# Kernel tuning notes

Measured on AMD Instinct MI355X. Metric: run time of the kernel, lower is better.

Reference implementation:

```python
import jax, jax.numpy as jnp
import numpy as np


def _forward(q, k, Wq, bq, Wk, bk, Wp, bp, eps=1e-4):
    b, ck, hk, wk, dk = k.shape
    n = hk * wk * dk                      # k sequence length == per-block q tokens
    # k branch: flatten spatial, project 256 -> 32
    kf = jnp.einsum('bci,cd->bid', k.reshape(b, ck, n), Wk) + bk   # (b, n, C)
    k_norm = jnp.linalg.norm(kf, axis=1)                           # (b, C): norm over positions (torch dim=1)
    c = q.shape[1]
    hq, wq, dq = q.shape[2], q.shape[3], q.shape[4]
    Nq = hq * wq * dq
    qf = jnp.einsum('bci,cd->bid', q.reshape(b, c, Nq), Wq) + bq   # (b, Nq, C)
    C = qf.shape[-1]
    Bh, Bw, Bd = hq // hk, wq // wk, dq // dk
    G = Bh * Bw * Bd
    # gather all (h_k, w_k, d_k) blocks: (b, G, n, C) -- replaces triple python loop
    qb = (qf.reshape(b, Bh, hk, Bw, wk, Bd, dk, C)
            .transpose(0, 1, 3, 5, 2, 4, 6, 7)
            .reshape(b, G, n, C))
    q_norm = jnp.linalg.norm(qb, axis=2)                           # (b, G, C): per-channel norm over block positions
    denom = jnp.einsum('bc,bgc->bg', k_norm, q_norm) + eps         # scalar per (batch, block)
    # sim[b,g,j,i] = <kf[b,i,:], qb[b,g,j,:]> / denom  (already in post-permute layout)
    sim = jnp.einsum('bic,bgjc->bgji', kf, qb) / denom[:, :, None, None]
    att = jax.nn.softmax(sim, axis=-1)                             # softmax over k positions i
    out = jnp.einsum('bgji,bgic->bgjc', att, qb)                   # (b, G, n, C)
    # min-max renorm over positions within each block (torch dim=1 of (b,n,C))
    mn = out.min(axis=2, keepdims=True)
    mx = out.max(axis=2, keepdims=True)
    v = (out - mn) / (mx - mn + eps)
    # faithful torch reshape: (b, C, n) row-major reinterpreted as (b, hk, wk, dk, C)
    v = v.transpose(0, 1, 3, 2).reshape(b, Bh, Bw, Bd, hk, wk, dk, C)
    # scatter blocks back to full volume
    v = v.transpose(0, 1, 4, 2, 5, 3, 6, 7).reshape(b, hq, wq, dq, C)
    out = jnp.einsum('bhwdc,ce->bhwde', v, Wp) + bp
    return out.transpose(0, 4, 1, 2, 3)                            # (b, C, hq, wq, dq)


def setup_inputs() -> dict:
    key = jax.random.key(0)
    ks = jax.random.split(key, 8)
    nf = 16
    q = jax.random.normal(ks[0], (2, nf * 2, 32, 32, 32), jnp.float32)
    k = jax.random.normal(ks[1], (2, nf * 16, 8, 8, 8), jnp.float32)
    Wq = jax.random.normal(ks[2], (nf * 2, nf * 2), jnp.float32) * 0.05
    bq = jax.random.normal(ks[3], (nf * 2,), jnp.float32) * 0.05
    Wk = jax.random.normal(ks[4], (nf * 16, nf * 2), jnp.float32) * 0.05
    bk = jax.random.normal(ks[5], (nf * 2,), jnp.float32) * 0.05
    Wp = jax.random.normal(ks[6], (nf * 2, nf * 2), jnp.float32) * 0.05
    bp = jax.random.normal(ks[7], (nf * 2,), jnp.float32) * 0.05
    return {"q": q, "k": k, "Wq": Wq, "bq": bq, "Wk": Wk, "bk": bk, "Wp": Wp, "bp": bp}


def reference(q, k, Wq, bq, Wk, bk, Wp, bp):
    return _forward(q, k, Wq, bq, Wk, bk, Wp, bp)
```

## Files before the change

kernel.cpp:

```cpp
#include <hip/hip_runtime.h>
#include <hip/hip_bf16.h>
#include <cstdint>

typedef __attribute__((ext_vector_type(8))) short bf16x8;
typedef __attribute__((ext_vector_type(4))) float f32x4;

static __device__ __forceinline__ float lo16(uint32_t u){ return __uint_as_float(u << 16); }
static __device__ __forceinline__ float hi16(uint32_t u){ return __uint_as_float(u & 0xffff0000u); }
static __device__ __forceinline__ uint32_t f2bf(float x){
    uint32_t u = __float_as_uint(x);
    return (u + 0x7fffu + ((u >> 16) & 1u)) >> 16;
}
static __device__ __forceinline__ uint32_t pack2(float a, float b){
    return f2bf(a) | (f2bf(b) << 16);
}

__global__ __launch_bounds__(1024) void k_kf(const float* __restrict__ k,
    const float* __restrict__ Wk, const float* __restrict__ bk,
    uint32_t* __restrict__ kf_pack)
{
    __shared__ float Wk_s[8192];
    __shared__ float bk_s[32];
    __shared__ float red[32][32];
    int t = threadIdx.x;
    for (int L = t; L < 8192; L += 1024) Wk_s[L] = Wk[L];
    if (t < 32) bk_s[t] = bk[t];
    __syncthreads();
    int blk = blockIdx.x;
    int b = blk >> 7, i0 = (blk & 127) * 4;
    int d = t & 31, sub = t >> 5;
    int i = i0 + (sub >> 3);
    int cp = sub & 7;
    const float* kb = k + (size_t)b * 131072;
    float acc = 0.f;
    #pragma unroll 8
    for (int cc = 0; cc < 32; ++cc){
        int c = cp*32 + cc;
        acc += kb[c*512 + i] * Wk_s[c*32 + d];
    }
    red[sub][d] = acc;
    __syncthreads();
    if (t < 128){
        int isel = t >> 5, dd = t & 31;
        float s = bk_s[dd];
        #pragma unroll
        for (int cp2 = 0; cp2 < 8; ++cp2) s += red[isel*8 + cp2][dd];
        float sO = __shfl_xor(s, 1, 64);
        if ((dd & 1) == 0)
            kf_pack[(b*512 + i0 + isel)*16 + (dd >> 1)] = pack2(s, sO);
    }
}

__global__ __launch_bounds__(1024) void k_qb(const float* __restrict__ q,
    const float* __restrict__ Wq, const float* __restrict__ bq,
    uint32_t* __restrict__ qb_pack)
{
    __shared__ float Wq_s[1024], bq_s[32], q_s[8192];
    int t = threadIdx.x;
    int blk = blockIdx.x;
    int bg = blk >> 1, h = blk & 1;
    int b = bg >> 6, g = bg & 63;
    int bh = g >> 4, bw = (g >> 2) & 3, bd = g & 3;
    Wq_s[t & 1023] = Wq[t & 1023];
    if (t < 32) bq_s[t] = bq[t];
    const float* qbase = q + (size_t)b * 1048576;
    #pragma unroll
    for (int m = 0; m < 2; ++m){
        int L4 = m*1024 + t;
        int f4 = L4 & 1, iw = (L4 >> 1) & 7, ihl = (L4 >> 4) & 3, c = L4 >> 6;
        const float* src = qbase + c*32768 + (bh*8 + h*4 + ihl)*1024
                         + (bw*8 + iw)*32 + bd*8 + f4*4;
        float4 v = *(const float4*)src;
        *(float4*)&q_s[c*256 + ihl*64 + iw*8 + f4*4] = v;
    }
    __syncthreads();
    int d = t & 31, sub = t >> 5;
    uint32_t* qb_out = qb_pack + (size_t)bg * 8192 + h*4096;
    for (int it = 0; it < 8; ++it){
        int jl = it*32 + sub;
        float acc = bq_s[d];
        #pragma unroll
        for (int c = 0; c < 32; ++c)
            acc += q_s[c*256 + jl] * Wq_s[c*32 + d];
        float accO = __shfl_xor(acc, 1, 64);
        if ((d & 1) == 0) qb_out[jl*16 + (d >> 1)] = pack2(acc, accO);
    }
}

__global__ __launch_bounds__(1024) void k_attn_mfma(const uint32_t* __restrict__ kf_pack,
    const uint32_t* __restrict__ qb_pack,
    float* __restrict__ oraw, float* __restrict__ mnp, float* __restrict__ mxp)
{
    __shared__ uint32_t kfs32[8192];
    __shared__ uint16_t qbV16[16384];
    __shared__ uint16_t Ps16[16384];
    __shared__ float mred[16][64];
    __shared__ float stat[64][32];
    __shared__ float dens[16][16];
    __shared__ float knsh[32], vssh[32], dsh[32];
    __shared__ float denom_s;
    int t = threadIdx.x;
    int blk = blockIdx.x;
    int bg = blk >> 1, jhalf = blk & 1;
    int b = bg >> 6;
    {
        const uint32_t* src = kf_pack + b*8192;
        #pragma unroll
        for (int m = 0; m < 8; ++m){
            int flat = m*1024 + t;
            uint32_t v = src[flat];
            int i = flat >> 4, dp = flat & 15;
            kfs32[i*16 + (((dp>>2) ^ (i&3)) & 3)*4 + (dp&3)] = v;
        }
    }
    {
        const uint32_t* src = qb_pack + (size_t)bg*8192;
        #pragma unroll
        for (int m = 0; m < 8; ++m){
            int flat = m*1024 + t;
            int i = flat >> 4, dp = flat & 15;
            uint32_t v = src[flat];
            int d0 = 2*dp, d1 = 2*dp + 1;
            qbV16[d0*512 + (((i>>3) ^ (d0&7)) & 63)*8 + (i&7)] = (uint16_t)(v & 0xffffu);
            qbV16[d1*512 + (((i>>3) ^ (d1&7)) & 63)*8 + (i&7)] = (uint16_t)(v >> 16);
        }
    }
    __syncthreads();
    {
        int dp = t & 15, ig = t >> 4;
        float lo2 = 0.f, hi2 = 0.f;
        #pragma unroll
        for (int ii = 0; ii < 8; ++ii){
            int i = ig*8 + ii;
            uint32_t u = kfs32[i*16 + (((dp>>2) ^ (i&3)) & 3)*4 + (dp&3)];
            float a = lo16(u), c = hi16(u);
            lo2 += a*a; hi2 += c*c;
        }
        stat[ig][dp*2] = lo2; stat[ig][dp*2+1] = hi2;
    }
    __syncthreads();
    if (t < 32){
        float s = 0.f;
        #pragma unroll
        for (int u = 0; u < 64; ++u) s += stat[u][t];
        knsh[t] = s;
    }
    __syncthreads();
    {
        int d = t & 31, ig = t >> 5;
        float q2 = 0.f, vs = 0.f;
        #pragma unroll
        for (int ii = 0; ii < 16; ii += 2){
            int i = ig*16 + ii;
            uint32_t u = *(__shared__ uint32_t*)&qbV16[d*512 + (((i>>3) ^ (d&7)) & 63)*8 + (i&7)];
            float a = lo16(u), c = hi16(u);
            q2 += a*a + c*c; vs += a + c;
        }
        stat[ig][d] = q2; stat[32 + ig][d] = vs;
    }
    __syncthreads();
    if (t < 32){
        float q2 = 0.f, vs = 0.f;
        #pragma unroll
        for (int u = 0; u < 32; ++u){ q2 += stat[u][t]; vs += stat[32+u][t]; }
        vssh[t] = vs;
        dsh[t] = sqrtf(knsh[t]) * sqrtf(q2);
    }
    __syncthreads();
    if (t == 0){
        float s = 0.f;
        #pragma unroll
        for (int d2 = 0; d2 < 32; ++d2) s += dsh[d2];
        denom_s = s + 1e-4f;
    }
    __syncthreads();
    float rden = 1.0f / denom_s;
    int wave = t >> 6, lane = t & 63;
    int ln15 = lane & 15, quad = lane >> 4;
    uint16_t* Pw = Ps16 + wave*1024;
    float vs0[4], vs1[4];
    #pragma unroll
    for (int r = 0; r < 4; ++r){
        vs0[r] = vssh[quad*4 + r];
        vs1[r] = vssh[16 + quad*4 + r];
    }
    float* obase = oraw + (size_t)bg * 16384;
    int jloc = wave*16 + ln15;
    int jglob = jhalf*256 + jloc;
    union { bf16x8 v; uint16_t u[8]; } afr;
    #pragma unroll
    for (int jj = 0; jj < 8; ++jj){
        int d = quad*8 + jj;
        afr.u[jj] = qbV16[d*512 + (((jglob>>3) ^ (d&7)) & 63)*8 + (jglob&7)];
    }
    f32x4 pv0 = {0.f,0.f,0.f,0.f}, pv1 = {0.f,0.f,0.f,0.f};
    float pdn[4] = {0.f,0.f,0.f,0.f};
    for (int sb = 0; sb < 4; ++sb){
        f32x4 sacc[8];
        #pragma unroll
        for (int u = 0; u < 8; ++u){
            int i = sb*128 + u*16 + ln15;
            bf16x8 bfr = *(__shared__ bf16x8*)&kfs32[i*16 + ((quad ^ (i&3)) & 3)*4];
            f32x4 z = {0.f,0.f,0.f,0.f};
            sacc[u] = __builtin_amdgcn_mfma_f32_16x16x32_bf16(afr.v, bfr, z, 0, 0, 0);
        }
        #pragma unroll
        for (int h2 = 0; h2 < 2; ++h2){
            #pragma unroll
            for (int u4 = 0; u4 < 4; ++u4){
                int u = h2*4 + u4;
                int il = u4*16 + ln15;
                #pragma unroll
                for (int r = 0; r < 4; ++r){
                    float x = sacc[u][r] * rden;
                    float e = x + x*x*(0.5f + x*(1.0f/6.0f));
                    pdn[r] += e;
                    int jrow = quad*4 + r;
                    Pw[jrow*64 + (((il>>3) ^ (jrow&3)) & 7)*8 + (il&7)] = (uint16_t)f2bf(e);
                }
            }
            __threadfence_block();
            #pragma unroll
            for (int ks = 0; ks < 2; ++ks){
                int i0 = ks*32 + quad*8;
                bf16x8 bp = *(__shared__ bf16x8*)&Pw[ln15*64 + (((i0>>3) ^ (ln15&3)) & 7)*8];
                int ig = sb*128 + h2*64 + i0;
                int c0 = ln15, c1 = 16 + ln15;
                bf16x8 av0 = *(__shared__ bf16x8*)&qbV16[c0*512 + (((ig>>3) ^ (c0&7)) & 63)*8];
                bf16x8 av1 = *(__shared__ bf16x8*)&qbV16[c1*512 + (((ig>>3) ^ (c1&7)) & 63)*8];
                pv0 = __builtin_amdgcn_mfma_f32_16x16x32_bf16(av0, bp, pv0, 0, 0, 0);
                pv1 = __builtin_amdgcn_mfma_f32_16x16x32_bf16(av1, bp, pv1, 0, 0, 0);
            }
        }
    }
    #pragma unroll
    for (int r = 0; r < 4; ++r){
        float s = pdn[r];
        s += __shfl_xor(s, 1, 64);
        s += __shfl_xor(s, 2, 64);
        s += __shfl_xor(s, 4, 64);
        s += __shfl_xor(s, 8, 64);
        if (ln15 == 0) dens[wave][quad*4 + r] = s;
    }
    __threadfence_block();
    float rl = 1.0f / (512.f + dens[wave][ln15]);
    float o0[4], o1[4];
    #pragma unroll
    for (int r = 0; r < 4; ++r){
        o0[r] = (vs0[r] + pv0[r]) * rl;
        o1[r] = (vs1[r] + pv1[r]) * rl;
        obase[(quad*4 + r)*512 + jglob]      = o0[r];
        obase[(16 + quad*4 + r)*512 + jglob] = o1[r];
    }
    #pragma unroll
    for (int r = 0; r < 4; ++r){
        float mnA = o0[r], mxA = o0[r], mnB = o1[r], mxB = o1[r];
        #pragma unroll
        for (int off = 1; off < 16; off <<= 1){
            mnA = fminf(mnA, __shfl_xor(mnA, off, 64));
            mxA = fmaxf(mxA, __shfl_xor(mxA, off, 64));
            mnB = fminf(mnB, __shfl_xor(mnB, off, 64));
            mxB = fmaxf(mxB, __shfl_xor(mxB, off, 64));
        }
        if (ln15 == 0){
            mred[wave][quad*4 + r]      = mnA;
            mred[wave][32 + quad*4 + r] = mxA;
            mred[wave][16 + quad*4 + r] = mnB;
            mred[wave][48 + quad*4 + r] = mxB;
        }
    }
    __syncthreads();
    if (t < 32){
        float mn = 3e38f, mx = -3e38f;
        #pragma unroll
        for (int w = 0; w < 16; ++w){
            mn = fminf(mn, mred[w][t]);
            mx = fmaxf(mx, mred[w][32 + t]);
        }
        int slot = (bg*2 + jhalf)*32 + t;
        mnp[slot] = mn;
        mxp[slot] = mx;
    }
}

__global__ __launch_bounds__(256) void k_proj(const float* __restrict__ oraw,
    const float* __restrict__ mnp, const float* __restrict__ mxp,
    const float* __restrict__ Wp, const float* __restrict__ bp,
    float* __restrict__ out)
{
    __shared__ float Wp_s[1024], bp_s[32];
    __shared__ float sh_v[32][32];
    __shared__ float sh_o[32][33];
    int t = threadIdx.x;
    if (t < 32) bp_s[t] = bp[t];
    for (int L = t; L < 1024; L += 256) Wp_s[L] = Wp[L];
    int blk = blockIdx.x;
    int b = blk >> 10, p0 = (blk & 1023) * 32;
    int c = t & 31, ip0 = t >> 5;
    float vv[4];
    #pragma unroll
    for (int m = 0; m < 4; ++m){
        int p = p0 + m*8 + ip0;
        int h = p >> 10, w = (p >> 5) & 31, dsp = p & 31;
        int f = (h >> 3)*262144 + (w >> 3)*65536 + (dsp >> 3)*16384
              + (h & 7)*2048 + (w & 7)*256 + (dsp & 7)*32;
        int flat = f + c;
        int cidx = b*2048 + (flat >> 9);
        int s0 = ((cidx >> 5) << 6) + (cidx & 31);
        float o  = oraw[(size_t)b*1048576 + flat];
        float mn = fminf(mnp[s0], mnp[s0 + 32]);
        float mx = fmaxf(mxp[s0], mxp[s0 + 32]);
        vv[m] = (o - mn) / (mx - mn + 1e-4f);
    }
    __syncthreads();
    #pragma unroll
    for (int m = 0; m < 4; ++m) sh_v[m*8 + ip0][c] = vv[m];
    __syncthreads();
    #pragma unroll
    for (int m = 0; m < 4; ++m){
        int pos = m*8 + ip0;
        float acc = bp_s[c];
        #pragma unroll
        for (int cc = 0; cc < 32; ++cc)
            acc += sh_v[pos][cc] * Wp_s[cc*32 + c];
        sh_o[pos][c] = acc;
    }
    __syncthreads();
    #pragma unroll
    for (int m = 0; m < 4; ++m){
        int e = m*8 + (t >> 5), pi = t & 31;
        out[((size_t)(b*32 + e) << 15) + p0 + pi] = sh_o[pi][e];
    }
}

extern "C" void kernel_launch(void* const* d_in, const int* in_sizes, int n_in,
                              void* d_out, int out_size, void* d_ws, size_t ws_size,
                              hipStream_t stream)
{
    const float* q  = (const float*)d_in[0];
    const float* k  = (const float*)d_in[1];
    const float* Wq = (const float*)d_in[2];
    const float* bq = (const float*)d_in[3];
    const float* Wk = (const float*)d_in[4];
    const float* bk = (const float*)d_in[5];
    const float* Wp = (const float*)d_in[6];
    const float* bp = (const float*)d_in[7];

    float* base      = (float*)d_ws;
    uint32_t* kf_pack = (uint32_t*)base;
    uint32_t* qb_pack = (uint32_t*)(base + 16384);
    float* oraw      = base + 1064960;
    float* mnp       = base + 3162112;
    float* mxp       = base + 3170304;
    float* outp      = (float*)d_out;

    hipLaunchKernelGGL(k_kf,        dim3(256),  dim3(1024), 0, stream, k, Wk, bk, kf_pack);
    hipLaunchKernelGGL(k_qb,        dim3(256),  dim3(1024), 0, stream, q, Wq, bq, qb_pack);
    hipLaunchKernelGGL(k_attn_mfma, dim3(256),  dim3(1024), 0, stream, kf_pack, qb_pack, oraw, mnp, mxp);
    hipLaunchKernelGGL(k_proj,      dim3(2048), dim3(256), 0, stream, oraw, mnp, mxp, Wp, bp, outp);
}
```

Measured before the change: 127.4 us.

## Merge projection kernels, keep softmax probabilities in registers via permlane swaps, split attention finer

The separate k and q projection kernels are merged into one launch that branches on block index. The q projection caches Wq columns in registers and computes four positions per thread. In attention, the score MFMA operands are swapped so the exponentiated scores can be packed with v_cvt_pk_bf16_f32 and rearranged with permlane32/16 swaps straight into the B operand of the PV MFMA, dropping the LDS round-trip for P and its buffer. Attention now runs 512 blocks of 512 threads with four query quarters, so min/max partials grow to four slots and k_proj reduces over them. The cost is recomputing the k-norm and q statistics in twice as many blocks, and relying on gfx950-specific instructions.

```diff
diff --git a/kernel.cpp b/kernel.cpp
--- a/kernel.cpp
+++ b/kernel.cpp
@@ -14,100 +14,127 @@
 static __device__ __forceinline__ uint32_t pack2(float a, float b){
     return f2bf(a) | (f2bf(b) << 16);
 }
-
-__global__ __launch_bounds__(1024) void k_kf(const float* __restrict__ k,
+static __device__ __forceinline__ uint32_t cvtpk(float a, float b){
+    uint32_t r;
+    asm("v_cvt_pk_bf16_f32 %0, %1, %2" : "=v"(r) : "v"(a), "v"(b));
+    return r;
+}
+static __device__ __forceinline__ void pl32swap(uint32_t &x, uint32_t &y){
+    asm("v_permlane32_swap_b32 %0, %1" : "+v"(x), "+v"(y));
+}
+static __device__ __forceinline__ void pl16swap(uint32_t &x, uint32_t &y){
+    asm("v_permlane16_swap_b32 %0, %1" : "+v"(x), "+v"(y));
+}
+
+__global__ __launch_bounds__(1024) void k_pre(const float* __restrict__ q,
+    const float* __restrict__ k,
+    const float* __restrict__ Wq, const float* __restrict__ bq,
     const float* __restrict__ Wk, const float* __restrict__ bk,
-    uint32_t* __restrict__ kf_pack)
+    uint32_t* __restrict__ qb_pack, uint32_t* __restrict__ kf_pack)
 {
-    __shared__ float Wk_s[8192];
-    __shared__ float bk_s[32];
-    __shared__ float red[32][32];
-    int t = threadIdx.x;
-    for (int L = t; L < 8192; L += 1024) Wk_s[L] = Wk[L];
-    if (t < 32) bk_s[t] = bk[t];
-    __syncthreads();
-    int blk = blockIdx.x;
-    int b = blk >> 7, i0 = (blk & 127) * 4;
-    int d = t & 31, sub = t >> 5;
-    int i = i0 + (sub >> 3);
-    int cp = sub & 7;
-    const float* kb = k + (size_t)b * 131072;
-    float acc = 0.f;
-    #pragma unroll 8
-    for (int cc = 0; cc < 32; ++cc){
-        int c = cp*32 + cc;
-        acc += kb[c*512 + i] * Wk_s[c*32 + d];
-    }
-    red[sub][d] = acc;
-    __syncthreads();
-    if (t < 128){
-        int isel = t >> 5, dd = t & 31;
-        float s = bk_s[dd];
-        #pragma unroll
-        for (int cp2 = 0; cp2 < 8; ++cp2) s += red[isel*8 + cp2][dd];
-        float sO = __shfl_xor(s, 1, 64);
-        if ((dd & 1) == 0)
-            kf_pack[(b*512 + i0 + isel)*16 + (dd >> 1)] = pack2(s, sO);
-    }
-}
-
-__global__ __launch_bounds__(1024) void k_qb(const float* __restrict__ q,
-    const float* __restrict__ Wq, const float* __restrict__ bq,
-    uint32_t* __restrict__ qb_pack)
-{
-    __shared__ float Wq_s[1024], bq_s[32], q_s[8192];
+    __shared__ float buf[9248];
     int t = threadIdx.x;
     int blk = blockIdx.x;
-    int bg = blk >> 1, h = blk & 1;
-    int b = bg >> 6, g = bg & 63;
-    int bh = g >> 4, bw = (g >> 2) & 3, bd = g & 3;
-    Wq_s[t & 1023] = Wq[t & 1023];
-    if (t < 32) bq_s[t] = bq[t];
-    const float* qbase = q + (size_t)b * 1048576;
-    #pragma unroll
-    for (int m = 0; m < 2; ++m){
-        int L4 = m*1024 + t;
-        int f4 = L4 & 1, iw = (L4 >> 1) & 7, ihl = (L4 >> 4) & 3, c = L4 >> 6;
-        const float* src = qbase + c*32768 + (bh*8 + h*4 + ihl)*1024
-                         + (bw*8 + iw)*32 + bd*8 + f4*4;
-        float4 v = *(const float4*)src;
-        *(float4*)&q_s[c*256 + ihl*64 + iw*8 + f4*4] = v;
-    }
-    __syncthreads();
-    int d = t & 31, sub = t >> 5;
-    uint32_t* qb_out = qb_pack + (size_t)bg * 8192 + h*4096;
-    for (int it = 0; it < 8; ++it){
-        int jl = it*32 + sub;
-        float acc = bq_s[d];
-        #pragma unroll
-        for (int c = 0; c < 32; ++c)
-            acc += q_s[c*256 + jl] * Wq_s[c*32 + d];
-        float accO = __shfl_xor(acc, 1, 64);
-        if ((d & 1) == 0) qb_out[jl*16 + (d >> 1)] = pack2(acc, accO);
-    }
-}
-
-__global__ __launch_bounds__(1024) void k_attn_mfma(const uint32_t* __restrict__ kf_pack,
+    if (blk < 256){
+        float* Wq_s = buf;
+        float* bq_s = buf + 1024;
+        float* q_s  = buf + 1056;
+        int bg = blk >> 1, h = blk & 1;
+        int b = bg >> 6, g = bg & 63;
+        int bh = g >> 4, bw = (g >> 2) & 3, bd = g & 3;
+        Wq_s[t] = Wq[t];
+        if (t < 32) bq_s[t] = bq[t];
+        const float* qbase = q + (size_t)b * 1048576;
+        #pragma unroll
+        for (int m = 0; m < 2; ++m){
+            int L4 = m*1024 + t;
+            int f4 = L4 & 1, iw = (L4 >> 1) & 7, ihl = (L4 >> 4) & 3, c = L4 >> 6;
+            const float* src = qbase + c*32768 + (bh*8 + h*4 + ihl)*1024
+                             + (bw*8 + iw)*32 + bd*8 + f4*4;
+            float4 v = *(const float4*)src;
+            *(float4*)&q_s[c*256 + ihl*64 + iw*8 + f4*4] = v;
+        }
+        __syncthreads();
+        int d = t & 31, sub = t >> 5;
+        float wq[32];
+        #pragma unroll
+        for (int c = 0; c < 32; ++c) wq[c] = Wq_s[c*32 + d];
+        uint32_t* qb_out = qb_pack + (size_t)bg * 8192 + h*4096;
+        #pragma unroll
+        for (int it = 0; it < 2; ++it){
+            int jl = it*128 + sub*4;
+            float bb = bq_s[d];
+            float a0 = bb, a1 = bb, a2 = bb, a3 = bb;
+            #pragma unroll
+            for (int c = 0; c < 32; ++c){
+                float4 qv = *(const float4*)&q_s[c*256 + jl];
+                a0 += qv.x * wq[c];
+                a1 += qv.y * wq[c];
+                a2 += qv.z * wq[c];
+                a3 += qv.w * wq[c];
+            }
+            float b0 = __shfl_xor(a0, 1, 64), b1 = __shfl_xor(a1, 1, 64);
+            float b2 = __shfl_xor(a2, 1, 64), b3 = __shfl_xor(a3, 1, 64);
+            if ((d & 1) == 0){
+                int w0 = d >> 1;
+                qb_out[(jl+0)*16 + w0] = pack2(a0, b0);
+                qb_out[(jl+1)*16 + w0] = pack2(a1, b1);
+                qb_out[(jl+2)*16 + w0] = pack2(a2, b2);
+                qb_out[(jl+3)*16 + w0] = pack2(a3, b3);
+            }
+        }
+    } else {
+        float* Wk_s = buf;
+        float* bk_s = buf + 8192;
+        float* red  = buf + 8224;
+        for (int L = t; L < 8192; L += 1024) Wk_s[L] = Wk[L];
+        if (t < 32) bk_s[t] = bk[t];
+        __syncthreads();
+        int kb_blk = blk - 256;
+        int b = kb_blk >> 7, i0 = (kb_blk & 127) * 4;
+        int d = t & 31, sub = t >> 5;
+        int i = i0 + (sub >> 3);
+        int cp = sub & 7;
+        const float* kbp = k + (size_t)b * 131072;
+        float acc = 0.f;
+        #pragma unroll 8
+        for (int cc = 0; cc < 32; ++cc){
+            int c = cp*32 + cc;
+            acc += kbp[c*512 + i] * Wk_s[c*32 + d];
+        }
+        red[sub*32 + d] = acc;
+        __syncthreads();
+        if (t < 128){
+            int isel = t >> 5, dd = t & 31;
+            float s = bk_s[dd];
+            #pragma unroll
+            for (int cp2 = 0; cp2 < 8; ++cp2) s += red[(isel*8 + cp2)*32 + dd];
+            float sO = __shfl_xor(s, 1, 64);
+            if ((dd & 1) == 0)
+                kf_pack[(b*512 + i0 + isel)*16 + (dd >> 1)] = pack2(s, sO);
+        }
+    }
+}
+
+__global__ __launch_bounds__(512) void k_attn_mfma(const uint32_t* __restrict__ kf_pack,
     const uint32_t* __restrict__ qb_pack,
     float* __restrict__ oraw, float* __restrict__ mnp, float* __restrict__ mxp)
 {
     __shared__ uint32_t kfs32[8192];
     __shared__ uint16_t qbV16[16384];
-    __shared__ uint16_t Ps16[16384];
-    __shared__ float mred[16][64];
-    __shared__ float stat[64][32];
-    __shared__ float dens[16][16];
+    __shared__ float mred[8][64];
+    __shared__ float stat[32][32];
     __shared__ float knsh[32], vssh[32], dsh[32];
     __shared__ float denom_s;
     int t = threadIdx.x;
     int blk = blockIdx.x;
-    int bg = blk >> 1, jhalf = blk & 1;
+    int bg = blk >> 2, jq = blk & 3;
     int b = bg >> 6;
     {
         const uint32_t* src = kf_pack + b*8192;
         #pragma unroll
-        for (int m = 0; m < 8; ++m){
-            int flat = m*1024 + t;
+        for (int m = 0; m < 16; ++m){
+            int flat = m*512 + t;
             uint32_t v = src[flat];
             int i = flat >> 4, dp = flat & 15;
             kfs32[i*16 + (((dp>>2) ^ (i&3)) & 3)*4 + (dp&3)] = v;
@@ -116,8 +143,8 @@
     {
         const uint32_t* src = qb_pack + (size_t)bg*8192;
         #pragma unroll
-        for (int m = 0; m < 8; ++m){
-            int flat = m*1024 + t;
+        for (int m = 0; m < 16; ++m){
+            int flat = m*512 + t;
             int i = flat >> 4, dp = flat & 15;
             uint32_t v = src[flat];
             int d0 = 2*dp, d1 = 2*dp + 1;
@@ -130,8 +157,8 @@
         int dp = t & 15, ig = t >> 4;
         float lo2 = 0.f, hi2 = 0.f;
         #pragma unroll
-        for (int ii = 0; ii < 8; ++ii){
-            int i = ig*8 + ii;
+        for (int ii = 0; ii < 16; ++ii){
+            int i = ig*16 + ii;
             uint32_t u = kfs32[i*16 + (((dp>>2) ^ (i&3)) & 3)*4 + (dp&3)];
             float a = lo16(u), c = hi16(u);
             lo2 += a*a; hi2 += c*c;
@@ -142,7 +169,7 @@
     if (t < 32){
         float s = 0.f;
         #pragma unroll
-        for (int u = 0; u < 64; ++u) s += stat[u][t];
+        for (int u = 0; u < 32; ++u) s += stat[u][t];
         knsh[t] = s;
     }
     __syncthreads();
@@ -150,19 +177,19 @@
         int d = t & 31, ig = t >> 5;
         float q2 = 0.f, vs = 0.f;
         #pragma unroll
-        for (int ii = 0; ii < 16; ii += 2){
-            int i = ig*16 + ii;
+        for (int ii = 0; ii < 32; ii += 2){
+            int i = ig*32 + ii;
             uint32_t u = *(__shared__ uint32_t*)&qbV16[d*512 + (((i>>3) ^ (d&7)) & 63)*8 + (i&7)];
             float a = lo16(u), c = hi16(u);
             q2 += a*a + c*c; vs += a + c;
         }
-        stat[ig][d] = q2; stat[32 + ig][d] = vs;
+        stat[ig][d] = q2; stat[16 + ig][d] = vs;
     }
     __syncthreads();
     if (t < 32){
         float q2 = 0.f, vs = 0.f;
         #pragma unroll
-        for (int u = 0; u < 32; ++u){ q2 += stat[u][t]; vs += stat[32+u][t]; }
+        for (int u = 0; u < 16; ++u){ q2 += stat[u][t]; vs += stat[16+u][t]; }
         vssh[t] = vs;
         dsh[t] = sqrtf(knsh[t]) * sqrtf(q2);
     }
@@ -177,7 +204,6 @@
     float rden = 1.0f / denom_s;
     int wave = t >> 6, lane = t & 63;
     int ln15 = lane & 15, quad = lane >> 4;
-    uint16_t* Pw = Ps16 + wave*1024;
     float vs0[4], vs1[4];
     #pragma unroll
     for (int r = 0; r < 4; ++r){
@@ -185,72 +211,62 @@
         vs1[r] = vssh[16 + quad*4 + r];
     }
     float* obase = oraw + (size_t)bg * 16384;
-    int jloc = wave*16 + ln15;
-    int jglob = jhalf*256 + jloc;
+    int jloc = jq*128 + wave*16 + ln15;
     union { bf16x8 v; uint16_t u[8]; } afr;
     #pragma unroll
     for (int jj = 0; jj < 8; ++jj){
         int d = quad*8 + jj;
-        afr.u[jj] = qbV16[d*512 + (((jglob>>3) ^ (d&7)) & 63)*8 + (jglob&7)];
+        afr.u[jj] = qbV16[d*512 + (((jloc>>3) ^ (d&7)) & 63)*8 + (jloc&7)];
     }
     f32x4 pv0 = {0.f,0.f,0.f,0.f}, pv1 = {0.f,0.f,0.f,0.f};
-    float pdn[4] = {0.f,0.f,0.f,0.f};
+    float pdn = 0.f;
     for (int sb = 0; sb < 4; ++sb){
-        f32x4 sacc[8];
-        #pragma unroll
-        for (int u = 0; u < 8; ++u){
-            int i = sb*128 + u*16 + ln15;
-            bf16x8 bfr = *(__shared__ bf16x8*)&kfs32[i*16 + ((quad ^ (i&3)) & 3)*4];
+        #pragma unroll
+        for (int ch = 0; ch < 4; ++ch){
+            int ib = sb*128 + ch*32;
+            int i0 = ib + ln15;
+            int i1 = i0 + 16;
+            bf16x8 k0 = *(__shared__ bf16x8*)&kfs32[i0*16 + ((quad ^ (i0&3)) & 3)*4];
+            bf16x8 k1 = *(__shared__ bf16x8*)&kfs32[i1*16 + ((quad ^ (i1&3)) & 3)*4];
             f32x4 z = {0.f,0.f,0.f,0.f};
-            sacc[u] = __builtin_amdgcn_mfma_f32_16x16x32_bf16(afr.v, bfr, z, 0, 0, 0);
-        }
-        #pragma unroll
-        for (int h2 = 0; h2 < 2; ++h2){
+            f32x4 s0 = __builtin_amdgcn_mfma_f32_16x16x32_bf16(k0, afr.v, z, 0, 0, 0);
+            f32x4 s1 = __builtin_amdgcn_mfma_f32_16x16x32_bf16(k1, afr.v, z, 0, 0, 0);
+            float e0[4], e1[4];
             #pragma unroll
-            for (int u4 = 0; u4 < 4; ++u4){
-                int u = h2*4 + u4;
-                int il = u4*16 + ln15;
-                #pragma unroll
-                for (int r = 0; r < 4; ++r){
-                    float x = sacc[u][r] * rden;
-                    float e = x + x*x*(0.5f + x*(1.0f/6.0f));
-                    pdn[r] += e;
-                    int jrow = quad*4 + r;
-                    Pw[jrow*64 + (((il>>3) ^ (jrow&3)) & 7)*8 + (il&7)] = (uint16_t)f2bf(e);
-                }
+            for (int r = 0; r < 4; ++r){
+                float x = s0[r] * rden;
+                e0[r] = x + x*x*(0.5f + x*(1.0f/6.0f));
+                pdn += e0[r];
+                x = s1[r] * rden;
+                e1[r] = x + x*x*(0.5f + x*(1.0f/6.0f));
+                pdn += e1[r];
             }
-            __threadfence_block();
-            #pragma unroll
-            for (int ks = 0; ks < 2; ++ks){
-                int i0 = ks*32 + quad*8;
-                bf16x8 bp = *(__shared__ bf16x8*)&Pw[ln15*64 + (((i0>>3) ^ (ln15&3)) & 7)*8];
-                int ig = sb*128 + h2*64 + i0;
-                int c0 = ln15, c1 = 16 + ln15;
-                bf16x8 av0 = *(__shared__ bf16x8*)&qbV16[c0*512 + (((ig>>3) ^ (c0&7)) & 63)*8];
-                bf16x8 av1 = *(__shared__ bf16x8*)&qbV16[c1*512 + (((ig>>3) ^ (c1&7)) & 63)*8];
-                pv0 = __builtin_amdgcn_mfma_f32_16x16x32_bf16(av0, bp, pv0, 0, 0, 0);
-                pv1 = __builtin_amdgcn_mfma_f32_16x16x32_bf16(av1, bp, pv1, 0, 0, 0);
-            }
-        }
-    }
-    #pragma unroll
-    for (int r = 0; r < 4; ++r){
-        float s = pdn[r];
-        s += __shfl_xor(s, 1, 64);
-        s += __shfl_xor(s, 2, 64);
-        s += __shfl_xor(s, 4, 64);
-        s += __shfl_xor(s, 8, 64);
-        if (ln15 == 0) dens[wave][quad*4 + r] = s;
-    }
-    __threadfence_block();
-    float rl = 1.0f / (512.f + dens[wave][ln15]);
+            uint32_t A0 = cvtpk(e0[0], e0[1]);
+            uint32_t A1 = cvtpk(e0[2], e0[3]);
+            uint32_t B0 = cvtpk(e1[0], e1[1]);
+            uint32_t B1 = cvtpk(e1[2], e1[3]);
+            pl32swap(A0, B0); pl16swap(A0, B0);
+            pl32swap(A1, B1); pl16swap(A1, B1);
+            union { bf16x8 v; uint32_t w[4]; } bp;
+            bp.w[0] = A0; bp.w[1] = A1; bp.w[2] = B0; bp.w[3] = B1;
+            int ig = ib + quad*8;
+            int c0 = ln15, c1 = 16 + ln15;
+            bf16x8 av0 = *(__shared__ bf16x8*)&qbV16[c0*512 + (((ig>>3) ^ (c0&7)) & 63)*8];
+            bf16x8 av1 = *(__shared__ bf16x8*)&qbV16[c1*512 + (((ig>>3) ^ (c1&7)) & 63)*8];
+            pv0 = __builtin_amdgcn_mfma_f32_16x16x32_bf16(av0, bp.v, pv0, 0, 0, 0);
+            pv1 = __builtin_amdgcn_mfma_f32_16x16x32_bf16(av1, bp.v, pv1, 0, 0, 0);
+        }
+    }
+    pdn += __shfl_xor(pdn, 16, 64);
+    pdn += __shfl_xor(pdn, 32, 64);
+    float rl = 1.0f / (512.f + pdn);
     float o0[4], o1[4];
     #pragma unroll
     for (int r = 0; r < 4; ++r){
         o0[r] = (vs0[r] + pv0[r]) * rl;
         o1[r] = (vs1[r] + pv1[r]) * rl;
-        obase[(quad*4 + r)*512 + jglob]      = o0[r];
-        obase[(16 + quad*4 + r)*512 + jglob] = o1[r];
+        obase[(quad*4 + r)*512 + jloc]      = o0[r];
+        obase[(16 + quad*4 + r)*512 + jloc] = o1[r];
     }
     #pragma unroll
     for (int r = 0; r < 4; ++r){
@@ -273,11 +289,11 @@
     if (t < 32){
         float mn = 3e38f, mx = -3e38f;
         #pragma unroll
-        for (int w = 0; w < 16; ++w){
+        for (int w = 0; w < 8; ++w){
             mn = fminf(mn, mred[w][t]);
             mx = fmaxf(mx, mred[w][32 + t]);
         }
-        int slot = (bg*2 + jhalf)*32 + t;
+        int slot = (bg*4 + jq)*32 + t;
         mnp[slot] = mn;
         mxp[slot] = mx;
     }
@@ -306,10 +322,10 @@
               + (h & 7)*2048 + (w & 7)*256 + (dsp & 7)*32;
         int flat = f + c;
         int cidx = b*2048 + (flat >> 9);
-        int s0 = ((cidx >> 5) << 6) + (cidx & 31);
+        int s0 = ((cidx >> 5) << 7) + (cidx & 31);
         float o  = oraw[(size_t)b*1048576 + flat];
-        float mn = fminf(mnp[s0], mnp[s0 + 32]);
-        float mx = fmaxf(mxp[s0], mxp[s0 + 32]);
+        float mn = fminf(fminf(mnp[s0], mnp[s0 + 32]), fminf(mnp[s0 + 64], mnp[s0 + 96]));
+        float mx = fmaxf(fmaxf(mxp[s0], mxp[s0 + 32]), fmaxf(mxp[s0 + 64], mxp[s0 + 96]));
         vv[m] = (o - mn) / (mx - mn + 1e-4f);
     }
     __syncthreads();
@@ -351,11 +367,10 @@
     uint32_t* qb_pack = (uint32_t*)(base + 16384);
     float* oraw      = base + 1064960;
     float* mnp       = base + 3162112;
-    float* mxp       = base + 3170304;
+    float* mxp       = base + 3178496;
     float* outp      = (float*)d_out;
 
-    hipLaunchKernelGGL(k_kf,        dim3(256),  dim3(1024), 0, stream, k, Wk, bk, kf_pack);
-    hipLaunchKernelGGL(k_qb,        dim3(256),  dim3(1024), 0, stream, q, Wq, bq, qb_pack);
-    hipLaunchKernelGGL(k_attn_mfma, dim3(256),  dim3(1024), 0, stream, kf_pack, qb_pack, oraw, mnp, mxp);
-    hipLaunchKernelGGL(k_proj,      dim3(2048), dim3(256), 0, stream, oraw, mnp, mxp, Wp, bp, outp);
-}
+    hipLaunchKernelGGL(k_pre,       dim3(512),  dim3(1024), 0, stream, q, k, Wq, bq, Wk, bk, qb_pack, kf_pack);
+    hipLaunchKernelGGL(k_attn_mfma, dim3(512),  dim3(512),  0, stream, kf_pack, qb_pack, oraw, mnp, mxp);
+    hipLaunchKernelGGL(k_proj,      dim3(2048), dim3(256),  0, stream, oraw, mnp, mxp, Wp, bp, outp);
+}
```

Result: faster. 110.2 us (-13.5%).
